# Kernel tuning notes

Hardware: AMD Instinct MI355X
Metric: run time of the kernel (lower is better)

Reference implementation:

```python
import jax, jax.numpy as jnp
import numpy as np
from jax import lax

EPS = 0.05 ** 2        # geomloss: eps = blur**p with p=2
N_ITERS = 50           # fixed log-domain Sinkhorn iterations (converged regime)
W_MSE = 1.0
W_OT = 1.0


def _sqcost(x, y):
    # x: (B,T,C), y: (B,S,C) -> (B,T,S) cost C_ij = 0.5*||x_i - y_j||^2
    x2 = jnp.sum(x * x, axis=-1)                      # (B,T)
    y2 = jnp.sum(y * y, axis=-1)                      # (B,S)
    xy = jnp.einsum('btc,bsc->bts', x, y)             # (B,T,S)
    return 0.5 * (x2[:, :, None] + y2[:, None, :] - 2.0 * xy)


def _softmin(C, h, logw):
    # -eps * logsumexp_j( logw + (h_j - C_ij)/eps );  C:(B,T,S), h:(B,S) -> (B,T)
    return -EPS * jax.nn.logsumexp(logw + (h[:, None, :] - C) / EPS, axis=-1)


def _sinkhorn_divergence(x, y):
    # Debiased entropic Sinkhorn divergence with uniform weights, per batch. (B,)
    B, T, _ = x.shape
    S = y.shape[1]
    loga = -np.float32(np.log(T))
    logb = -np.float32(np.log(S))
    C_xy = _sqcost(x, y)          # (B,T,S)
    C_xx = _sqcost(x, x)          # (B,T,T)
    C_yy = _sqcost(y, y)          # (B,S,S)
    C_yx = jnp.swapaxes(C_xy, 1, 2)

    f = jnp.zeros((B, T), x.dtype)   # potential on x for OT(x,y)
    g = jnp.zeros((B, S), x.dtype)   # potential on y for OT(x,y)
    p = jnp.zeros((B, T), x.dtype)   # symmetric potential for OT(x,x)
    q = jnp.zeros((B, S), x.dtype)   # symmetric potential for OT(y,y)

    @jax.checkpoint
    def step(carry, _):
        f, g, p, q = carry
        f1 = _softmin(C_xy, g, logb)
        g1 = _softmin(C_yx, f, loga)
        p1 = _softmin(C_xx, p, loga)
        q1 = _softmin(C_yy, q, logb)
        # averaged (stabilized) updates, as in geomloss symmetric Sinkhorn
        return (0.5 * (f + f1), 0.5 * (g + g1), 0.5 * (p + p1), 0.5 * (q + q1)), None

    (f, g, p, q), _ = lax.scan(step, (f, g, p, q), None, length=N_ITERS)
    # S_eps(a,b) = <a, f - p> + <b, g - q>  with uniform a, b
    return jnp.mean(f - p, axis=1) + jnp.mean(g - q, axis=1)


def setup_inputs() -> dict:
    key = jax.random.key(0)
    k1, k2 = jax.random.split(key)
    B, T, C = 8, 1024, 16
    pred = jax.random.normal(k1, (B, T, C), dtype=jnp.float32)
    gt = jax.random.normal(k2, (B, T, C), dtype=jnp.float32)
    return {"pred_sequence": pred, "gt_sequence": gt}


def reference(pred_sequence, gt_sequence):
    mse_loss = jnp.mean((pred_sequence - gt_sequence) ** 2)
    ot_loss = jnp.mean(_sinkhorn_divergence(pred_sequence, gt_sequence))
    total = W_MSE * mse_loss + W_OT * ot_loss
    return jnp.stack([total, mse_loss, ot_loss])  # (total, mse, ot)
```

## Files before the change

### kernel.cpp

```cpp
#include <hip/hip_runtime.h>
#include <hip/hip_fp16.h>

#define NN 1024
#define BATCH 8
#define CDIM 16
#define NITER 38
#define CAPC 512
#define CAPF 256

static constexpr float K_SCALE = 577.0780163555854f;
static constexpr float EPS_LN2 = 0.0017328679513998632f;
static constexpr float MARGIN_T = 1.1f * 577.0780163555854f;
static constexpr float MARGIN_C = 4.0f * 577.0780163555854f;

#if __has_builtin(__builtin_amdgcn_exp2f)
#define EXP2F(x) __builtin_amdgcn_exp2f(x)
#else
#define EXP2F(x) exp2f(x)
#endif
#if __has_builtin(__builtin_amdgcn_logf)
#define LOG2F(x) __builtin_amdgcn_logf(x)
#else
#define LOG2F(x) log2f(x)
#endif

__device__ __half g_C16[4][BATCH][NN][NN];
__device__ float g_pot[2][4][BATCH][NN];
__device__ float g_mse_part[8];
__device__ __align__(16) unsigned g_cand_c[4 * BATCH * NN * CAPC];
__device__ unsigned g_cnt_c[4 * BATCH * NN];
__device__ __align__(16) unsigned g_cand_f[4 * BATCH * NN * CAPF];
__device__ unsigned g_cnt_f[4 * BATCH * NN];

struct alignas(8) H4 { __half2 a, b; };

__global__ __launch_bounds__(256) void cost_kernel(const float* __restrict__ x,
                                                   const float* __restrict__ y) {
    int bid = blockIdx.x;
    int m = bid >> 9;
    int b = (bid >> 6) & 7;
    int ig = bid & 63;
    const float* X = (m == 1 || m == 3) ? y : x;
    const float* Y = (m == 0 || m == 3) ? y : x;
    int tid = threadIdx.x;
    int j0 = tid * 4;

    if (m == 0) {
        int lid = bid & 511;
        if (tid < 64) (&g_pot[0][0][0][0])[lid * 64 + tid] = 0.0f;
    }

    __shared__ float xs[16 * CDIM];
    __shared__ float x2s[16];
    xs[tid] = X[(size_t)(b * NN + ig * 16) * CDIM + tid];
    __syncthreads();
    if (tid < 16) {
        float a = 0.0f;
        #pragma unroll
        for (int k = 0; k < CDIM; ++k) a = fmaf(xs[tid * CDIM + k], xs[tid * CDIM + k], a);
        x2s[tid] = 0.5f * a;
    }

    float yr[4][16];
    const float4* Y4 = reinterpret_cast<const float4*>(Y + (size_t)(b * NN + j0) * CDIM);
    #pragma unroll
    for (int rr = 0; rr < 4; ++rr) {
        #pragma unroll
        for (int q = 0; q < 4; ++q) {
            float4 v = Y4[rr * 4 + q];
            yr[rr][q * 4 + 0] = v.x; yr[rr][q * 4 + 1] = v.y;
            yr[rr][q * 4 + 2] = v.z; yr[rr][q * 4 + 3] = v.w;
        }
    }
    float y2h[4];
    #pragma unroll
    for (int rr = 0; rr < 4; ++rr) {
        float acc = 0.0f;
        #pragma unroll
        for (int k = 0; k < CDIM; ++k) acc = fmaf(yr[rr][k], yr[rr][k], acc);
        y2h[rr] = 0.5f * acc;
    }
    __syncthreads();

    #pragma unroll 1
    for (int r = 0; r < 16; ++r) {
        float xv[CDIM];
        #pragma unroll
        for (int k = 0; k < CDIM; ++k) xv[k] = xs[r * CDIM + k];
        float x2h = x2s[r];

        float acc[4];
        #pragma unroll
        for (int rr = 0; rr < 4; ++rr) {
            float a = x2h + y2h[rr];
            #pragma unroll
            for (int k = 0; k < CDIM; ++k) a = fmaf(xv[k], -yr[rr][k], a);
            acc[rr] = a;
        }
        H4 out;
        out.a = __floats2half2_rn(acc[0], acc[1]);
        out.b = __floats2half2_rn(acc[2], acc[3]);
        int i = ig * 16 + r;
        *reinterpret_cast<H4*>(&g_C16[m][b][i][j0]) = out;
    }

    if (m == 0 && ig == 0) {
        const float4* xa = reinterpret_cast<const float4*>(x + (size_t)b * NN * CDIM);
        const float4* ya = reinterpret_cast<const float4*>(y + (size_t)b * NN * CDIM);
        float acc = 0.0f;
        for (int e = tid; e < NN * CDIM / 4; e += 256) {
            float4 xv = xa[e], yv = ya[e];
            float d0 = xv.x - yv.x, d1 = xv.y - yv.y;
            float d2 = xv.z - yv.z, d3 = xv.w - yv.w;
            acc = fmaf(d0, d0, acc); acc = fmaf(d1, d1, acc);
            acc = fmaf(d2, d2, acc); acc = fmaf(d3, d3, acc);
        }
        #pragma unroll
        for (int off = 32; off; off >>= 1) acc += __shfl_xor(acc, off, 64);
        __shared__ float red[4];
        int lane = tid & 63, wid = tid >> 6;
        if (lane == 0) red[wid] = acc;
        __syncthreads();
        if (tid == 0) g_mse_part[b] = red[0] + red[1] + red[2] + red[3];
    }
}

__device__ inline float2 cvt2(unsigned int u) {
    __half2 h;
    *reinterpret_cast<unsigned int*>(&h) = u;
    return __half22float2(h);
}

template <bool BUILD>
__global__ __launch_bounds__(256) void iter_kernel_t(int parity) {
    int bid = blockIdx.x;
    int p = bid >> 9;
    int b = (bid >> 6) & 7;
    int rg = bid & 63;
    int hsel = (p == 0) ? 1 : (p == 1) ? 0 : p;

    int tid = threadIdx.x;
    int lane = tid & 63, wid = tid >> 6;

    const float* __restrict__ hin  = g_pot[parity][hsel][b];
    const float* __restrict__ oldp = g_pot[parity][p][b];
    float* __restrict__ outp       = g_pot[parity ^ 1][p][b];

    float hs[16];
    {
        const float4* h4 = reinterpret_cast<const float4*>(hin);
        float4 a0 = h4[lane * 2], a1 = h4[lane * 2 + 1];
        float4 b0 = h4[128 + lane * 2], b1 = h4[128 + lane * 2 + 1];
        hs[0] = a0.x * K_SCALE;  hs[1] = a0.y * K_SCALE;
        hs[2] = a0.z * K_SCALE;  hs[3] = a0.w * K_SCALE;
        hs[4] = a1.x * K_SCALE;  hs[5] = a1.y * K_SCALE;
        hs[6] = a1.z * K_SCALE;  hs[7] = a1.w * K_SCALE;
        hs[8]  = b0.x * K_SCALE; hs[9]  = b0.y * K_SCALE;
        hs[10] = b0.z * K_SCALE; hs[11] = b0.w * K_SCALE;
        hs[12] = b1.x * K_SCALE; hs[13] = b1.y * K_SCALE;
        hs[14] = b1.z * K_SCALE; hs[15] = b1.w * K_SCALE;
    }

    #pragma unroll
    for (int r = 0; r < 4; ++r) {
        int i = rg * 16 + wid * 4 + r;
        const uint4* crow = reinterpret_cast<const uint4*>(&g_C16[p][b][i][0]);
        uint4 ca = crow[lane];
        uint4 cb = crow[64 + lane];

        float t[16];
        {
            float2 f;
            f = cvt2(ca.x); t[0] = fmaf(f.x, -K_SCALE, hs[0]);  t[1] = fmaf(f.y, -K_SCALE, hs[1]);
            f = cvt2(ca.y); t[2] = fmaf(f.x, -K_SCALE, hs[2]);  t[3] = fmaf(f.y, -K_SCALE, hs[3]);
            f = cvt2(ca.z); t[4] = fmaf(f.x, -K_SCALE, hs[4]);  t[5] = fmaf(f.y, -K_SCALE, hs[5]);
            f = cvt2(ca.w); t[6] = fmaf(f.x, -K_SCALE, hs[6]);  t[7] = fmaf(f.y, -K_SCALE, hs[7]);
            f = cvt2(cb.x); t[8] = fmaf(f.x, -K_SCALE, hs[8]);  t[9] = fmaf(f.y, -K_SCALE, hs[9]);
            f = cvt2(cb.y); t[10] = fmaf(f.x, -K_SCALE, hs[10]); t[11] = fmaf(f.y, -K_SCALE, hs[11]);
            f = cvt2(cb.z); t[12] = fmaf(f.x, -K_SCALE, hs[12]); t[13] = fmaf(f.y, -K_SCALE, hs[13]);
            f = cvt2(cb.w); t[14] = fmaf(f.x, -K_SCALE, hs[14]); t[15] = fmaf(f.y, -K_SCALE, hs[15]);
        }

        float mx = t[0];
        #pragma unroll
        for (int k = 1; k < 16; ++k) mx = fmaxf(mx, t[k]);
        #pragma unroll
        for (int off = 32; off; off >>= 1) mx = fmaxf(mx, __shfl_xor(mx, off, 64));

        float s = 0.0f;
        #pragma unroll
        for (int k = 0; k < 16; ++k) s += EXP2F(t[k] - mx);
        #pragma unroll
        for (int off = 32; off; off >>= 1) s += __shfl_xor(s, off, 64);

        if (lane == 0) {
            float res = -EPS_LN2 * (mx - 10.0f + LOG2F(s));
            outp[i] = 0.5f * (oldp[i] + res);
        }

        if (BUILD) {
            size_t rowid = (size_t)((p * BATCH + b) * NN + i);
            float thr = mx - MARGIN_C;
            int c = 0;
            #pragma unroll
            for (int k = 0; k < 16; ++k) c += (t[k] >= thr) ? 1 : 0;
            int incl = c;
            #pragma unroll
            for (int off = 1; off < 64; off <<= 1) {
                int v = __shfl_up(incl, off, 64);
                if (lane >= off) incl += v;
            }
            int excl = incl - c;
            int total = __shfl(incl, 63, 64);
            if (lane == 0) g_cnt_c[rowid] = (unsigned)(total < CAPC ? total : CAPC);

            union U4 { uint4 q; unsigned w[4]; } A, B2;
            A.q = ca; B2.q = cb;
            unsigned* dst = &g_cand_c[rowid * CAPC];
            int slot = excl;
            #pragma unroll
            for (int k = 0; k < 16; ++k) {
                if (t[k] >= thr) {
                    if (slot < CAPC) {
                        unsigned hb = (k < 8) ? A.w[k >> 1] : B2.w[(k - 8) >> 1];
                        hb = (hb >> ((k & 1) * 16)) & 0xffffu;
                        unsigned j = (k < 8) ? (unsigned)(lane * 8 + k)
                                             : (unsigned)(512 + lane * 8 + (k - 8));
                        dst[slot] = (j << 16) | hb;
                    }
                    ++slot;
                }
            }
        }
    }
}

template <bool BUILDF, bool COARSE_SRC>
__global__ __launch_bounds__(256) void sparse_iter_t(int parity) {
    int bid = blockIdx.x;
    int p = bid >> 7;
    int b = (bid >> 4) & 7;
    int rg = bid & 15;
    int hsel = (p == 0) ? 1 : (p == 1) ? 0 : p;

    const float* __restrict__ hin  = g_pot[parity][hsel][b];
    const float* __restrict__ oldp = g_pot[parity][p][b];
    float* __restrict__ outp       = g_pot[parity ^ 1][p][b];

    __shared__ float h2[NN];
    {
        const float4* h4 = reinterpret_cast<const float4*>(hin);
        float4 v = h4[threadIdx.x];
        v.x *= K_SCALE; v.y *= K_SCALE; v.z *= K_SCALE; v.w *= K_SCALE;
        reinterpret_cast<float4*>(h2)[threadIdx.x] = v;
    }
    __syncthreads();

    int tid = threadIdx.x;
    int lane = tid & 63, wid = tid >> 6;
    int c = lane & 3;
    int i = rg * 64 + wid * 16 + (lane >> 2);
    size_t rowid = (size_t)((p * BATCH + b) * NN + i);

    const unsigned* __restrict__ candsrc = COARSE_SRC ? g_cand_c : g_cand_f;
    const int cap = COARSE_SRC ? CAPC : CAPF;
    int cnt = (int)(COARSE_SRC ? g_cnt_c[rowid] : g_cnt_f[rowid]);
    const uint4* __restrict__ cd4 =
        reinterpret_cast<const uint4*>(candsrc + rowid * cap);

    float m = -3.0e38f;
    float s = 0.0f;
    int nstep = (cnt + 15) >> 4;
    for (int k = 0; k < nstep; ++k) {
        int base = k * 16 + c * 4;
        uint4 u = cd4[k * 4 + c];
        __half hh;
        *reinterpret_cast<unsigned short*>(&hh) = (unsigned short)(u.x & 0xffffu);
        float t0 = fmaf(__half2float(hh), -K_SCALE, h2[(u.x >> 16) & 1023]);
        *reinterpret_cast<unsigned short*>(&hh) = (unsigned short)(u.y & 0xffffu);
        float t1 = fmaf(__half2float(hh), -K_SCALE, h2[(u.y >> 16) & 1023]);
        *reinterpret_cast<unsigned short*>(&hh) = (unsigned short)(u.z & 0xffffu);
        float t2 = fmaf(__half2float(hh), -K_SCALE, h2[(u.z >> 16) & 1023]);
        *reinterpret_cast<unsigned short*>(&hh) = (unsigned short)(u.w & 0xffffu);
        float t3 = fmaf(__half2float(hh), -K_SCALE, h2[(u.w >> 16) & 1023]);
        t0 = (base + 0 < cnt) ? t0 : -3.0e38f;
        t1 = (base + 1 < cnt) ? t1 : -3.0e38f;
        t2 = (base + 2 < cnt) ? t2 : -3.0e38f;
        t3 = (base + 3 < cnt) ? t3 : -3.0e38f;
        float sm = fmaxf(fmaxf(t0, t1), fmaxf(t2, t3));
        float nm = fmaxf(m, sm);
        s = s * EXP2F(m - nm) + EXP2F(t0 - nm) + EXP2F(t1 - nm)
                              + EXP2F(t2 - nm) + EXP2F(t3 - nm);
        m = nm;
    }
    #pragma unroll
    for (int off = 1; off <= 2; off <<= 1) {
        float m2 = __shfl_xor(m, off, 64);
        float s2 = __shfl_xor(s, off, 64);
        float nm = fmaxf(m, m2);
        s = s * EXP2F(m - nm) + s2 * EXP2F(m2 - nm);
        m = nm;
    }
    if (c == 0) {
        float res = -EPS_LN2 * (m - 10.0f + LOG2F(s));
        outp[i] = 0.5f * (oldp[i] + res);
    }

    if (BUILDF) {
        float thr = m - MARGIN_T;
        int cl = 0;
        for (int k = 0; k < nstep; ++k) {
            int base = k * 16 + c * 4;
            uint4 u = cd4[k * 4 + c];
            unsigned w[4] = {u.x, u.y, u.z, u.w};
            #pragma unroll
            for (int o = 0; o < 4; ++o) {
                if (base + o < cnt) {
                    __half hh;
                    *reinterpret_cast<unsigned short*>(&hh) = (unsigned short)(w[o] & 0xffffu);
                    float tv = fmaf(__half2float(hh), -K_SCALE, h2[(w[o] >> 16) & 1023]);
                    if (tv >= thr) ++cl;
                }
            }
        }
        int g0 = lane & ~3;
        int c0 = __shfl(cl, g0 + 0, 64);
        int c1 = __shfl(cl, g0 + 1, 64);
        int c2 = __shfl(cl, g0 + 2, 64);
        int c3 = __shfl(cl, g0 + 3, 64);
        int excl = ((c >= 1) ? c0 : 0) + ((c >= 2) ? c1 : 0) + ((c >= 3) ? c2 : 0);
        int total = c0 + c1 + c2 + c3;
        if (c == 0) g_cnt_f[rowid] = (unsigned)(total < CAPF ? total : CAPF);
        unsigned* dst = &g_cand_f[rowid * CAPF];
        int slot = excl;
        for (int k = 0; k < nstep; ++k) {
            int base = k * 16 + c * 4;
            uint4 u = cd4[k * 4 + c];
            unsigned w[4] = {u.x, u.y, u.z, u.w};
            #pragma unroll
            for (int o = 0; o < 4; ++o) {
                if (base + o < cnt) {
                    __half hh;
                    *reinterpret_cast<unsigned short*>(&hh) = (unsigned short)(w[o] & 0xffffu);
                    float tv = fmaf(__half2float(hh), -K_SCALE, h2[(w[o] >> 16) & 1023]);
                    if (tv >= thr) {
                        if (slot < CAPF) dst[slot] = w[o];
                        ++slot;
                    }
                }
            }
        }
    }
}

__global__ __launch_bounds__(256) void epilogue_kernel(float* __restrict__ out) {
    int tid = threadIdx.x;
    const float* f = &g_pot[0][0][0][0];
    const float* g = &g_pot[0][1][0][0];
    const float* pp = &g_pot[0][2][0][0];
    const float* q = &g_pot[0][3][0][0];
    float acc = 0.0f;
    for (int idx = tid; idx < BATCH * NN; idx += 256) {
        acc += (f[idx] - pp[idx]) + (g[idx] - q[idx]);
    }
    float macc = (tid < 8) ? g_mse_part[tid] : 0.0f;
    #pragma unroll
    for (int off = 32; off; off >>= 1) {
        acc += __shfl_xor(acc, off, 64);
        macc += __shfl_xor(macc, off, 64);
    }
    __shared__ float red[4], redm[4];
    int lane = tid & 63, wid = tid >> 6;
    if (lane == 0) { red[wid] = acc; redm[wid] = macc; }
    __syncthreads();
    if (tid == 0) {
        float ot = (red[0] + red[1] + red[2] + red[3]) / (float)(BATCH * NN);
        float mse = (redm[0] + redm[1] + redm[2] + redm[3]) / (float)(BATCH * NN * CDIM);
        out[0] = mse + ot;
        out[1] = mse;
        out[2] = ot;
    }
}

extern "C" void kernel_launch(void* const* d_in, const int* in_sizes, int n_in,
                              void* d_out, int out_size, void* d_ws, size_t ws_size,
                              hipStream_t stream) {
    const float* pred = (const float*)d_in[0];
    const float* gt   = (const float*)d_in[1];
    float* out = (float*)d_out;

    cost_kernel<<<4 * BATCH * 64, 256, 0, stream>>>(pred, gt);
    iter_kernel_t<true><<<4 * BATCH * 64, 256, 0, stream>>>(0);
    sparse_iter_t<false, true><<<512, 256, 0, stream>>>(1);
    sparse_iter_t<true, true><<<512, 256, 0, stream>>>(0);
    for (int t = 3; t < NITER; ++t) {
        sparse_iter_t<false, false><<<512, 256, 0, stream>>>(t & 1);
    }
    epilogue_kernel<<<1, 256, 0, stream>>>(out);
}
```

Baseline: 192.9 us.

## Fuse cost computation with first dense Sinkhorn iteration via shared-memory tile

```diff
diff --git a/kernel.cpp b/kernel.cpp
--- a/kernel.cpp
+++ b/kernel.cpp
@@ -24,7 +24,6 @@
 #define LOG2F(x) log2f(x)
 #endif
 
-__device__ __half g_C16[4][BATCH][NN][NN];
 __device__ float g_pot[2][4][BATCH][NN];
 __device__ float g_mse_part[8];
 __device__ __align__(16) unsigned g_cand_c[4 * BATCH * NN * CAPC];
@@ -34,8 +33,14 @@
 
 struct alignas(8) H4 { __half2 a, b; };
 
-__global__ __launch_bounds__(256) void cost_kernel(const float* __restrict__ x,
-                                                   const float* __restrict__ y) {
+__device__ inline float2 cvt2(unsigned int u) {
+    __half2 h;
+    *reinterpret_cast<unsigned int*>(&h) = u;
+    return __half22float2(h);
+}
+
+__global__ __launch_bounds__(256) void cost_t0_kernel(const float* __restrict__ x,
+                                                      const float* __restrict__ y) {
     int bid = blockIdx.x;
     int m = bid >> 9;
     int b = (bid >> 6) & 7;
@@ -43,15 +48,13 @@
     const float* X = (m == 1 || m == 3) ? y : x;
     const float* Y = (m == 0 || m == 3) ? y : x;
     int tid = threadIdx.x;
+    int lane = tid & 63, wid = tid >> 6;
     int j0 = tid * 4;
 
-    if (m == 0) {
-        int lid = bid & 511;
-        if (tid < 64) (&g_pot[0][0][0][0])[lid * 64 + tid] = 0.0f;
-    }
-
+    __shared__ __align__(16) __half tile[16][NN];
     __shared__ float xs[16 * CDIM];
     __shared__ float x2s[16];
+
     xs[tid] = X[(size_t)(b * NN + ig * 16) * CDIM + tid];
     __syncthreads();
     if (tid < 16) {
@@ -100,8 +103,80 @@
         H4 out;
         out.a = __floats2half2_rn(acc[0], acc[1]);
         out.b = __floats2half2_rn(acc[2], acc[3]);
-        int i = ig * 16 + r;
-        *reinterpret_cast<H4*>(&g_C16[m][b][i][j0]) = out;
+        *reinterpret_cast<H4*>(&tile[r][j0]) = out;
+    }
+    __syncthreads();
+
+    #pragma unroll 1
+    for (int r = 0; r < 4; ++r) {
+        int rloc = wid * 4 + r;
+        int i = ig * 16 + rloc;
+        const uint4* crow = reinterpret_cast<const uint4*>(&tile[rloc][0]);
+        uint4 ca = crow[lane];
+        uint4 cb = crow[64 + lane];
+
+        float t[16];
+        {
+            float2 f;
+            f = cvt2(ca.x); t[0] = f.x * -K_SCALE;  t[1] = f.y * -K_SCALE;
+            f = cvt2(ca.y); t[2] = f.x * -K_SCALE;  t[3] = f.y * -K_SCALE;
+            f = cvt2(ca.z); t[4] = f.x * -K_SCALE;  t[5] = f.y * -K_SCALE;
+            f = cvt2(ca.w); t[6] = f.x * -K_SCALE;  t[7] = f.y * -K_SCALE;
+            f = cvt2(cb.x); t[8] = f.x * -K_SCALE;  t[9] = f.y * -K_SCALE;
+            f = cvt2(cb.y); t[10] = f.x * -K_SCALE; t[11] = f.y * -K_SCALE;
+            f = cvt2(cb.z); t[12] = f.x * -K_SCALE; t[13] = f.y * -K_SCALE;
+            f = cvt2(cb.w); t[14] = f.x * -K_SCALE; t[15] = f.y * -K_SCALE;
+        }
+
+        float mx = t[0];
+        #pragma unroll
+        for (int k = 1; k < 16; ++k) mx = fmaxf(mx, t[k]);
+        #pragma unroll
+        for (int off = 32; off; off >>= 1) mx = fmaxf(mx, __shfl_xor(mx, off, 64));
+
+        float s = 0.0f;
+        #pragma unroll
+        for (int k = 0; k < 16; ++k) s += EXP2F(t[k] - mx);
+        #pragma unroll
+        for (int off = 32; off; off >>= 1) s += __shfl_xor(s, off, 64);
+
+        if (lane == 0) {
+            float res = -EPS_LN2 * (mx - 10.0f + LOG2F(s));
+            g_pot[1][m][b][i] = 0.5f * res;
+        }
+
+        size_t rowid = (size_t)((m * BATCH + b) * NN + i);
+        float thr = mx - MARGIN_C;
+        int c = 0;
+        #pragma unroll
+        for (int k = 0; k < 16; ++k) c += (t[k] >= thr) ? 1 : 0;
+        int incl = c;
+        #pragma unroll
+        for (int off = 1; off < 64; off <<= 1) {
+            int v = __shfl_up(incl, off, 64);
+            if (lane >= off) incl += v;
+        }
+        int excl = incl - c;
+        int total = __shfl(incl, 63, 64);
+        if (lane == 0) g_cnt_c[rowid] = (unsigned)(total < CAPC ? total : CAPC);
+
+        union U4 { uint4 q; unsigned w[4]; } A, B2;
+        A.q = ca; B2.q = cb;
+        unsigned* dst = &g_cand_c[rowid * CAPC];
+        int slot = excl;
+        #pragma unroll
+        for (int k = 0; k < 16; ++k) {
+            if (t[k] >= thr) {
+                if (slot < CAPC) {
+                    unsigned hb = (k < 8) ? A.w[k >> 1] : B2.w[(k - 8) >> 1];
+                    hb = (hb >> ((k & 1) * 16)) & 0xffffu;
+                    unsigned j = (k < 8) ? (unsigned)(lane * 8 + k)
+                                         : (unsigned)(512 + lane * 8 + (k - 8));
+                    dst[slot] = (j << 16) | hb;
+                }
+                ++slot;
+            }
+        }
     }
 
     if (m == 0 && ig == 0) {
@@ -118,120 +193,9 @@
         #pragma unroll
         for (int off = 32; off; off >>= 1) acc += __shfl_xor(acc, off, 64);
         __shared__ float red[4];
-        int lane = tid & 63, wid = tid >> 6;
         if (lane == 0) red[wid] = acc;
         __syncthreads();
         if (tid == 0) g_mse_part[b] = red[0] + red[1] + red[2] + red[3];
-    }
-}
-
-__device__ inline float2 cvt2(unsigned int u) {
-    __half2 h;
-    *reinterpret_cast<unsigned int*>(&h) = u;
-    return __half22float2(h);
-}
-
-template <bool BUILD>
-__global__ __launch_bounds__(256) void iter_kernel_t(int parity) {
-    int bid = blockIdx.x;
-    int p = bid >> 9;
-    int b = (bid >> 6) & 7;
-    int rg = bid & 63;
-    int hsel = (p == 0) ? 1 : (p == 1) ? 0 : p;
-
-    int tid = threadIdx.x;
-    int lane = tid & 63, wid = tid >> 6;
-
-    const float* __restrict__ hin  = g_pot[parity][hsel][b];
-    const float* __restrict__ oldp = g_pot[parity][p][b];
-    float* __restrict__ outp       = g_pot[parity ^ 1][p][b];
-
-    float hs[16];
-    {
-        const float4* h4 = reinterpret_cast<const float4*>(hin);
-        float4 a0 = h4[lane * 2], a1 = h4[lane * 2 + 1];
-        float4 b0 = h4[128 + lane * 2], b1 = h4[128 + lane * 2 + 1];
-        hs[0] = a0.x * K_SCALE;  hs[1] = a0.y * K_SCALE;
-        hs[2] = a0.z * K_SCALE;  hs[3] = a0.w * K_SCALE;
-        hs[4] = a1.x * K_SCALE;  hs[5] = a1.y * K_SCALE;
-        hs[6] = a1.z * K_SCALE;  hs[7] = a1.w * K_SCALE;
-        hs[8]  = b0.x * K_SCALE; hs[9]  = b0.y * K_SCALE;
-        hs[10] = b0.z * K_SCALE; hs[11] = b0.w * K_SCALE;
-        hs[12] = b1.x * K_SCALE; hs[13] = b1.y * K_SCALE;
-        hs[14] = b1.z * K_SCALE; hs[15] = b1.w * K_SCALE;
-    }
-
-    #pragma unroll
-    for (int r = 0; r < 4; ++r) {
-        int i = rg * 16 + wid * 4 + r;
-        const uint4* crow = reinterpret_cast<const uint4*>(&g_C16[p][b][i][0]);
-        uint4 ca = crow[lane];
-        uint4 cb = crow[64 + lane];
-
-        float t[16];
-        {
-            float2 f;
-            f = cvt2(ca.x); t[0] = fmaf(f.x, -K_SCALE, hs[0]);  t[1] = fmaf(f.y, -K_SCALE, hs[1]);
-            f = cvt2(ca.y); t[2] = fmaf(f.x, -K_SCALE, hs[2]);  t[3] = fmaf(f.y, -K_SCALE, hs[3]);
-            f = cvt2(ca.z); t[4] = fmaf(f.x, -K_SCALE, hs[4]);  t[5] = fmaf(f.y, -K_SCALE, hs[5]);
-            f = cvt2(ca.w); t[6] = fmaf(f.x, -K_SCALE, hs[6]);  t[7] = fmaf(f.y, -K_SCALE, hs[7]);
-            f = cvt2(cb.x); t[8] = fmaf(f.x, -K_SCALE, hs[8]);  t[9] = fmaf(f.y, -K_SCALE, hs[9]);
-            f = cvt2(cb.y); t[10] = fmaf(f.x, -K_SCALE, hs[10]); t[11] = fmaf(f.y, -K_SCALE, hs[11]);
-            f = cvt2(cb.z); t[12] = fmaf(f.x, -K_SCALE, hs[12]); t[13] = fmaf(f.y, -K_SCALE, hs[13]);
-            f = cvt2(cb.w); t[14] = fmaf(f.x, -K_SCALE, hs[14]); t[15] = fmaf(f.y, -K_SCALE, hs[15]);
-        }
-
-        float mx = t[0];
-        #pragma unroll
-        for (int k = 1; k < 16; ++k) mx = fmaxf(mx, t[k]);
-        #pragma unroll
-        for (int off = 32; off; off >>= 1) mx = fmaxf(mx, __shfl_xor(mx, off, 64));
-
-        float s = 0.0f;
-        #pragma unroll
-        for (int k = 0; k < 16; ++k) s += EXP2F(t[k] - mx);
-        #pragma unroll
-        for (int off = 32; off; off >>= 1) s += __shfl_xor(s, off, 64);
-
-        if (lane == 0) {
-            float res = -EPS_LN2 * (mx - 10.0f + LOG2F(s));
-            outp[i] = 0.5f * (oldp[i] + res);
-        }
-
-        if (BUILD) {
-            size_t rowid = (size_t)((p * BATCH + b) * NN + i);
-            float thr = mx - MARGIN_C;
-            int c = 0;
-            #pragma unroll
-            for (int k = 0; k < 16; ++k) c += (t[k] >= thr) ? 1 : 0;
-            int incl = c;
-            #pragma unroll
-            for (int off = 1; off < 64; off <<= 1) {
-                int v = __shfl_up(incl, off, 64);
-                if (lane >= off) incl += v;
-            }
-            int excl = incl - c;
-            int total = __shfl(incl, 63, 64);
-            if (lane == 0) g_cnt_c[rowid] = (unsigned)(total < CAPC ? total : CAPC);
-
-            union U4 { uint4 q; unsigned w[4]; } A, B2;
-            A.q = ca; B2.q = cb;
-            unsigned* dst = &g_cand_c[rowid * CAPC];
-            int slot = excl;
-            #pragma unroll
-            for (int k = 0; k < 16; ++k) {
-                if (t[k] >= thr) {
-                    if (slot < CAPC) {
-                        unsigned hb = (k < 8) ? A.w[k >> 1] : B2.w[(k - 8) >> 1];
-                        hb = (hb >> ((k & 1) * 16)) & 0xffffu;
-                        unsigned j = (k < 8) ? (unsigned)(lane * 8 + k)
-                                             : (unsigned)(512 + lane * 8 + (k - 8));
-                        dst[slot] = (j << 16) | hb;
-                    }
-                    ++slot;
-                }
-            }
-        }
     }
 }
 
@@ -389,8 +353,7 @@
     const float* gt   = (const float*)d_in[1];
     float* out = (float*)d_out;
 
-    cost_kernel<<<4 * BATCH * 64, 256, 0, stream>>>(pred, gt);
-    iter_kernel_t<true><<<4 * BATCH * 64, 256, 0, stream>>>(0);
+    cost_t0_kernel<<<4 * BATCH * 64, 256, 0, stream>>>(pred, gt);
     sparse_iter_t<false, true><<<512, 256, 0, stream>>>(1);
     sparse_iter_t<true, true><<<512, 256, 0, stream>>>(0);
     for (int t = 3; t < NITER; ++t) {
```

New measurement: 177.0 us. 1.09x faster.
